# Optimization experiments

Measured on AMD Instinct MI355X. Metric: run time of the kernel, lower is better.

Reference implementation:

```python
import jax, jax.numpy as jnp
import numpy as np

K = 3
PAD = 1
STRIDE = 1
DIL = 1


def _conv(x, w, b):
    # standard 3x3 conv, NCHW / OIHW
    y = jax.lax.conv_general_dilated(
        x, w, (STRIDE, STRIDE), [(PAD, PAD), (PAD, PAD)],
        rhs_dilation=(DIL, DIL),
        dimension_numbers=('NCHW', 'OIHW', 'NCHW'))
    return y + b[None, :, None, None]


def _deform_conv2d(x, offset, mask, weight, bias):
    # x: [B,C,H,W]; offset: [B,2*KK,Ho,Wo] (y,x interleaved per kernel tap);
    # mask: [B,KK,Ho,Wo]; weight: [Co,C,K,K]; bias: [Co]
    B, C, H, W = x.shape
    KK = K * K
    Ho, Wo = offset.shape[2], offset.shape[3]

    off = offset.reshape(B, KK, 2, Ho, Wo)
    dy, dx = off[:, :, 0], off[:, :, 1]          # [B,KK,Ho,Wo]

    ky, kx = jnp.meshgrid(jnp.arange(K), jnp.arange(K), indexing='ij')
    ky = ky.reshape(KK).astype(x.dtype)
    kx = kx.reshape(KK).astype(x.dtype)
    hs = (jnp.arange(Ho) * STRIDE - PAD).astype(x.dtype)
    ws = (jnp.arange(Wo) * STRIDE - PAD).astype(x.dtype)
    base_y = hs[None, :, None] + (ky * DIL)[:, None, None]   # [KK,Ho,1]
    base_x = ws[None, None, :] + (kx * DIL)[:, None, None]   # [KK,1,Wo]

    py = base_y[None] + dy                        # [B,KK,Ho,Wo] sample rows
    px = base_x[None] + dx                        # sample cols

    y0 = jnp.floor(py)
    x0 = jnp.floor(px)
    ly = py - y0                                  # bilinear fractional weights
    lx = px - x0
    y0i = y0.astype(jnp.int32)
    x0i = x0.astype(jnp.int32)

    flat = x.reshape(B, C, H * W)

    def gather(iy, ix):
        # zero-padded gather at integer locations -> [B,C,KK,Ho,Wo]
        valid = (iy >= 0) & (iy < H) & (ix >= 0) & (ix < W)
        iyc = jnp.clip(iy, 0, H - 1)
        ixc = jnp.clip(ix, 0, W - 1)
        idx = (iyc * W + ixc).reshape(B, 1, KK * Ho * Wo)
        g = jnp.take_along_axis(flat, jnp.broadcast_to(idx, (B, C, KK * Ho * Wo)), axis=2)
        g = g.reshape(B, C, KK, Ho, Wo)
        return g * valid[:, None].astype(x.dtype)

    val = (gather(y0i, x0i) * ((1 - ly) * (1 - lx))[:, None]
           + gather(y0i, x0i + 1) * ((1 - ly) * lx)[:, None]
           + gather(y0i + 1, x0i) * (ly * (1 - lx))[:, None]
           + gather(y0i + 1, x0i + 1) * (ly * lx)[:, None])

    val = val * mask[:, None]                     # DCNv2 modulation

    wr = weight.reshape(weight.shape[0], C, KK)   # [Co,C,KK]
    out = jnp.einsum('bckhw,ock->bohw', val, wr)
    return out + bias[None, :, None, None]


def setup_inputs() -> dict:
    key = jax.random.key(0)
    ks = jax.random.split(key, 7)
    B, C, Co, H, W = 4, 128, 256, 96, 96
    KK = K * K
    x = jax.random.normal(ks[0], (B, C, H, W), dtype=jnp.float32)
    weight = jax.random.normal(ks[1], (Co, C, K, K), dtype=jnp.float32) * 0.03
    bias = jax.random.normal(ks[2], (Co,), dtype=jnp.float32) * 0.01
    offset_w = jax.random.normal(ks[3], (2 * KK, C, K, K), dtype=jnp.float32) * 0.01
    offset_b = jax.random.normal(ks[4], (2 * KK,), dtype=jnp.float32) * 0.01
    mod_w = jax.random.normal(ks[5], (KK, C, K, K), dtype=jnp.float32) * 0.01
    mod_b = jnp.ones((KK,), dtype=jnp.float32)
    return {'x': x, 'weight': weight, 'bias': bias,
            'offset_w': offset_w, 'offset_b': offset_b,
            'mod_w': mod_w, 'mod_b': mod_b}


def reference(x, weight, bias, offset_w, offset_b, mod_w, mod_b):
    offset = _conv(x, offset_w, offset_b)
    mask = jax.nn.sigmoid(_conv(x, mod_w, mod_b))
    return _deform_conv2d(x, offset, mask, weight, bias)
```

## Files before the change

kernel.cpp:

```cpp
#include <hip/hip_runtime.h>
#include <math.h>

#define HH 96
#define WW 96
#define HW 9216
#define CIN 128
#define COUT 256

typedef _Float16 f16;
typedef _Float16 f16x2 __attribute__((ext_vector_type(2)));
typedef _Float16 f16x8 __attribute__((ext_vector_type(8)));
typedef __attribute__((ext_vector_type(4))) float f32x4;

static __device__ __forceinline__ unsigned short f2h(float f) {
  union { f16 h; unsigned short u; } v; v.h = (f16)f; return v.u;
}

__global__ __launch_bounds__(256) void k_prep(const float* __restrict__ x,
                                              const float* __restrict__ offw,
                                              const float* __restrict__ modw,
                                              const float* __restrict__ wgt,
                                              unsigned short* __restrict__ xTh,
                                              unsigned short* __restrict__ wAbF,
                                              unsigned short* __restrict__ wTtF) {
  __shared__ float tile[32][129];
  int bid = blockIdx.x;
  int t = threadIdx.x;
  if (bid < 1152) {
    int wseg = bid % 3, h = (bid / 3) % 96, b = bid / 288;
    int wl = t & 31, cg = t >> 5;
    const float* xp = x + ((size_t)(b * 128 + cg) * 96 + h) * 96 + wseg * 32 + wl;
#pragma unroll
    for (int i = 0; i < 16; ++i)
      tile[wl][cg + 8 * i] = xp[(size_t)8 * i * HW];
    __syncthreads();
    int cl = t & 127, wg = t >> 7;
    unsigned short* op = xTh + (((size_t)(b * 96 + h) * 96) + wseg * 32) * 128 + cl;
#pragma unroll
    for (int i = 0; i < 16; ++i)
      op[(size_t)(wg + 2 * i) * 128] = f2h(tile[wg + 2 * i][cl]);
  } else if (bid < 1296) {
    int i = (bid - 1152) * 256 + t;
    if (i < 9 * 2 * 4 * 512) {
      int j = i & 7;
      int l = (i >> 3) & 63;
      int ks = (i >> 9) & 3;
      int ng = i >> 11;
      int kpos = ng >> 1, n16 = ng & 1;
      int n = n16 * 16 + (l & 15);
      int c = ks * 32 + (l >> 4) * 8 + j;
      float v = 0.f;
      if (n < 18) v = offw[n * 1152 + c * 9 + kpos];
      else if (n < 27) v = modw[(n - 18) * 1152 + c * 9 + kpos];
      wAbF[i] = f2h(v);
    }
  } else {
    int i = (bid - 1296) * 256 + t;
    if (i < 9 * 16 * 4 * 512) {
      int j = i & 7;
      int l = (i >> 3) & 63;
      int ks = (i >> 9) & 3;
      int ng = i >> 11;
      int kpos = ng >> 4, n16 = ng & 15;
      int n = n16 * 16 + (l & 15);
      int c = ks * 32 + (l >> 4) * 8 + j;
      wTtF[i] = f2h(wgt[n * 1152 + c * 9 + kpos]);
    }
  }
}

__global__ __launch_bounds__(256) void k_main(const unsigned short* __restrict__ xTh,
                                              const unsigned short* __restrict__ wAbF,
                                              const unsigned short* __restrict__ wTtF,
                                              const float* __restrict__ offb,
                                              const float* __restrict__ modb,
                                              const float* __restrict__ bias,
                                              float* __restrict__ out) {
  __shared__ __align__(16) unsigned short Ab[64 * 72];
  __shared__ __align__(16) float ezs[4 * 1088];
  __shared__ float om_lds[27 * 65];

  int t = threadIdx.x;
  int l = t & 63;
  int w = t >> 6;
  int lm = l & 15, lq = l >> 4;
  int raw = blockIdx.x;
  int bid = (raw & 7) * 72 + (raw >> 3);
  int pix0 = bid * 64;
  int b = pix0 / HW;
  int posim0 = pix0 % HW;
  int ibase = b * HW;

  {
    int prow = pix0 + w * 16 + lm;
    int pimo = prow % HW;
    int hoo = pimo / 96, woo = pimo % 96;
    f32x4 acco[2];
    acco[0] = (f32x4){0.f, 0.f, 0.f, 0.f};
    acco[1] = (f32x4){0.f, 0.f, 0.f, 0.f};
    const f16x8 zv = {0, 0, 0, 0, 0, 0, 0, 0};
#pragma unroll 1
    for (int kpos = 0; kpos < 9; ++kpos) {
      int dyr = kpos / 3 - 1, dxr = kpos % 3 - 1;
      bool valid = ((unsigned)(hoo + dyr) < 96u) && ((unsigned)(woo + dxr) < 96u);
      int srow = valid ? (prow + dyr * 96 + dxr) : prow;
      const unsigned short* ap = xTh + (size_t)srow * 128 + lq * 8;
      const unsigned short* bp = wAbF + (size_t)(kpos * 8) * 512 + l * 8;
#pragma unroll
      for (int ks = 0; ks < 4; ++ks) {
        f16x8 af = valid ? *(const f16x8*)(ap + ks * 32) : zv;
        f16x8 bf0 = *(const f16x8*)(bp + (size_t)ks * 512);
        f16x8 bf1 = *(const f16x8*)(bp + (size_t)(4 + ks) * 512);
        acco[0] = __builtin_amdgcn_mfma_f32_16x16x32_f16(af, bf0, acco[0], 0, 0, 0);
        acco[1] = __builtin_amdgcn_mfma_f32_16x16x32_f16(af, bf1, acco[1], 0, 0, 0);
      }
    }
#pragma unroll
    for (int nt = 0; nt < 2; ++nt) {
      int n = nt * 16 + lm;
      if (n < 27) {
        float bv = (n < 18) ? offb[n] : modb[n - 18];
#pragma unroll
        for (int r = 0; r < 4; ++r) {
          float v = acco[nt][r] + bv;
          if (n >= 18) v = 1.f / (1.f + expf(-v));
          om_lds[n * 65 + w * 16 + lq * 4 + r] = v;
        }
      }
    }
  }
  __syncthreads();

  int px = t & 63;
  int basegrp = t >> 6;
  int pos = pix0 + px;
  int ho = (pos % HW) / 96, wo = pos % 96;

  f32x4 acc[4][4];
#pragma unroll
  for (int i = 0; i < 4; ++i)
#pragma unroll
    for (int j = 0; j < 4; ++j)
      acc[i][j] = (f32x4){0.f, 0.f, 0.f, 0.f};

  for (int kpos = 0; kpos < 9; ++kpos) {
    float dy = om_lds[(2 * kpos) * 65 + px];
    float dx = om_lds[(2 * kpos + 1) * 65 + px];
    float mk = om_lds[(18 + kpos) * 65 + px];
    float py = (float)(ho - 1 + kpos / 3) + dy;
    float pxf = (float)(wo - 1 + kpos % 3) + dx;
    float fy = floorf(py), fx = floorf(pxf);
    int y0 = (int)fy, x0 = (int)fx;
    float ly = py - fy, lx = pxf - fx;
    float w00 = (1.f - ly) * (1.f - lx), w01 = (1.f - ly) * lx;
    float w10 = ly * (1.f - lx),         w11 = ly * lx;
    bool vy0 = (unsigned)y0 < 96u, vy1 = (unsigned)(y0 + 1) < 96u;
    bool vx0 = (unsigned)x0 < 96u, vx1 = (unsigned)(x0 + 1) < 96u;
    w00 = (vy0 && vx0) ? w00 * mk : 0.f;
    w01 = (vy0 && vx1) ? w01 * mk : 0.f;
    w10 = (vy1 && vx0) ? w10 * mk : 0.f;
    w11 = (vy1 && vx1) ? w11 * mk : 0.f;
    int y0c = min(max(y0, 0), 95), y1c = min(max(y0 + 1, 0), 95);
    int x0c = min(max(x0, 0), 95), x1c = min(max(x0 + 1, 0), 95);
    int o00 = (ibase + y0c * 96 + x0c) * 128;
    int o01 = (ibase + y0c * 96 + x1c) * 128;
    int o10 = (ibase + y1c * 96 + x0c) * 128;
    int o11 = (ibase + y1c * 96 + x1c) * 128;
    f16 h00 = (f16)w00, h01 = (f16)w01, h10 = (f16)w10, h11 = (f16)w11;
    f16x2 wp00 = (f16x2){h00, h00}, wp01 = (f16x2){h01, h01};
    f16x2 wp10 = (f16x2){h10, h10}, wp11 = (f16x2){h11, h11};

#pragma unroll
    for (int half = 0; half < 2; ++half) {
      int c0 = half * 64;
      __syncthreads();
#pragma unroll
      for (int item = 0; item < 2; ++item) {
        int oct = basegrp + 4 * item;
        int cc = c0 + oct * 8;
        union { uint4 u; f16x2 h[4]; } a0, a1, a2, a3;
        a0.u = *(const uint4*)(xTh + o00 + cc);
        a1.u = *(const uint4*)(xTh + o01 + cc);
        a2.u = *(const uint4*)(xTh + o10 + cc);
        a3.u = *(const uint4*)(xTh + o11 + cc);
        union { f16x8 v; f16x2 h[4]; } r;
#pragma unroll
        for (int j = 0; j < 4; ++j)
          r.h[j] = a0.h[j] * wp00 + a1.h[j] * wp01 + a2.h[j] * wp10 + a3.h[j] * wp11;
        *(f16x8*)(Ab + px * 72 + oct * 8) = r.v;
      }
      __syncthreads();
#pragma unroll
      for (int ks = 0; ks < 2; ++ks) {
        f16x8 af[4], bfv[4];
#pragma unroll
        for (int mt = 0; mt < 4; ++mt)
          af[mt] = *(const f16x8*)(Ab + (mt * 16 + lm) * 72 + ks * 32 + lq * 8);
        const unsigned short* bp =
            wTtF + (size_t)((kpos * 16 + w * 4) * 4 + 2 * half + ks) * 512 + l * 8;
#pragma unroll
        for (int nt = 0; nt < 4; ++nt)
          bfv[nt] = *(const f16x8*)(bp + (size_t)nt * 4 * 512);
#pragma unroll
        for (int mt = 0; mt < 4; ++mt)
#pragma unroll
          for (int nt = 0; nt < 4; ++nt)
            acc[mt][nt] = __builtin_amdgcn_mfma_f32_16x16x32_f16(af[mt], bfv[nt], acc[mt][nt], 0, 0, 0);
      }
    }
  }

  float bias_v[4];
#pragma unroll
  for (int nt = 0; nt < 4; ++nt) bias_v[nt] = bias[w * 64 + nt * 16 + lm];
  float* ez = ezs + w * 1088;
#pragma unroll
  for (int nt = 0; nt < 4; ++nt) {
    __syncthreads();
#pragma unroll
    for (int mt = 0; mt < 4; ++mt)
#pragma unroll
      for (int r = 0; r < 4; ++r)
        ez[(mt * 16 + lq * 4 + r) * 17 + lm] = acc[mt][nt][r] + bias_v[nt];
    __syncthreads();
    float* ob = out + ((size_t)(b * COUT + w * 64 + nt * 16)) * HW + posim0;
#pragma unroll
    for (int j = 0; j < 16; ++j)
      ob[(size_t)j * HW + l] = ez[l * 17 + j];
  }
}

extern "C" void kernel_launch(void* const* d_in, const int* in_sizes, int n_in,
                              void* d_out, int out_size, void* d_ws, size_t ws_size,
                              hipStream_t stream) {
  const float* x      = (const float*)d_in[0];
  const float* weight = (const float*)d_in[1];
  const float* bias   = (const float*)d_in[2];
  const float* offw   = (const float*)d_in[3];
  const float* offb   = (const float*)d_in[4];
  const float* modw   = (const float*)d_in[5];
  const float* modb   = (const float*)d_in[6];
  float* out = (float*)d_out;
  float* ws = (float*)d_ws;

  unsigned short* xTh  = (unsigned short*)ws;
  unsigned short* wTtF = (unsigned short*)(ws + 2359296);
  unsigned short* wAbF = (unsigned short*)(ws + 2359296 + 147456);

  k_prep<<<2448, 256, 0, stream>>>(x, offw, modw, weight, xTh, wAbF, wTtF);
  k_main<<<576, 256, 0, stream>>>(xTh, wAbF, wTtF, offb, modb, bias, out);
}
```

Measured before the change: 185.1 us.

## Register-resident A fragments with prefetched bilinear gathers per wave

Each wave now owns 16 pixels and all 256 output channels, so it builds its own A fragments in registers from the bilinear gather instead of staging a shared 64-pixel tile in LDS behind block-wide barriers. The gathers for the next kernel tap are issued before the MFMAs of the current tap, which overlaps global latency with compute. The epilogue drops most of its barriers by using a per-wave LDS transpose region. In exchange, each wave loads the full weight tile from global memory, raising weight traffic and register pressure (16 accumulators plus 16 prefetch registers) under a 2-blocks-per-CU launch bound.

```diff
diff --git a/kernel.cpp b/kernel.cpp
--- a/kernel.cpp
+++ b/kernel.cpp
@@ -69,20 +69,18 @@
   }
 }
 
-__global__ __launch_bounds__(256) void k_main(const unsigned short* __restrict__ xTh,
-                                              const unsigned short* __restrict__ wAbF,
-                                              const unsigned short* __restrict__ wTtF,
-                                              const float* __restrict__ offb,
-                                              const float* __restrict__ modb,
-                                              const float* __restrict__ bias,
-                                              float* __restrict__ out) {
-  __shared__ __align__(16) unsigned short Ab[64 * 72];
-  __shared__ __align__(16) float ezs[4 * 1088];
+__global__ __launch_bounds__(256, 2) void k_main(const unsigned short* __restrict__ xTh,
+                                                 const unsigned short* __restrict__ wAbF,
+                                                 const unsigned short* __restrict__ wTtF,
+                                                 const float* __restrict__ offb,
+                                                 const float* __restrict__ modb,
+                                                 const float* __restrict__ bias,
+                                                 float* __restrict__ out) {
   __shared__ float om_lds[27 * 65];
+  __shared__ float ez[4 * 16 * 65];
 
   int t = threadIdx.x;
-  int l = t & 63;
-  int w = t >> 6;
+  int l = t & 63, w = t >> 6;
   int lm = l & 15, lq = l >> 4;
   int raw = blockIdx.x;
   int bid = (raw & 7) * 72 + (raw >> 3);
@@ -131,24 +129,24 @@
   }
   __syncthreads();
 
-  int px = t & 63;
-  int basegrp = t >> 6;
-  int pos = pix0 + px;
-  int ho = (pos % HW) / 96, wo = pos % 96;
-
-  f32x4 acc[4][4];
-#pragma unroll
-  for (int i = 0; i < 4; ++i)
-#pragma unroll
-    for (int j = 0; j < 4; ++j)
-      acc[i][j] = (f32x4){0.f, 0.f, 0.f, 0.f};
-
-  for (int kpos = 0; kpos < 9; ++kpos) {
-    float dy = om_lds[(2 * kpos) * 65 + px];
-    float dx = om_lds[(2 * kpos + 1) * 65 + px];
-    float mk = om_lds[(18 + kpos) * 65 + px];
-    float py = (float)(ho - 1 + kpos / 3) + dy;
-    float pxf = (float)(wo - 1 + kpos % 3) + dx;
+  int mypx = w * 16 + lm;
+  int pim = (pix0 + mypx) % HW;
+  int ho = pim / 96, wo = pim % 96;
+
+  f32x4 acc[16];
+#pragma unroll
+  for (int i = 0; i < 16; ++i) acc[i] = (f32x4){0.f, 0.f, 0.f, 0.f};
+
+  int o00 = 0, o01 = 0, o10 = 0, o11 = 0;
+  f16x2 wp00, wp01, wp10, wp11;
+  uint4 q00[4], q01[4], q10[4], q11[4];
+
+  auto geom_issue = [&](int kp) {
+    float dy = om_lds[(2 * kp) * 65 + mypx];
+    float dx = om_lds[(2 * kp + 1) * 65 + mypx];
+    float mk = om_lds[(18 + kp) * 65 + mypx];
+    float py = (float)(ho - 1 + kp / 3) + dy;
+    float pxf = (float)(wo - 1 + kp % 3) + dx;
     float fy = floorf(py), fx = floorf(pxf);
     int y0 = (int)fy, x0 = (int)fx;
     float ly = py - fy, lx = pxf - fx;
@@ -162,71 +160,71 @@
     w11 = (vy1 && vx1) ? w11 * mk : 0.f;
     int y0c = min(max(y0, 0), 95), y1c = min(max(y0 + 1, 0), 95);
     int x0c = min(max(x0, 0), 95), x1c = min(max(x0 + 1, 0), 95);
-    int o00 = (ibase + y0c * 96 + x0c) * 128;
-    int o01 = (ibase + y0c * 96 + x1c) * 128;
-    int o10 = (ibase + y1c * 96 + x0c) * 128;
-    int o11 = (ibase + y1c * 96 + x1c) * 128;
+    o00 = (ibase + y0c * 96 + x0c) * 128;
+    o01 = (ibase + y0c * 96 + x1c) * 128;
+    o10 = (ibase + y1c * 96 + x0c) * 128;
+    o11 = (ibase + y1c * 96 + x1c) * 128;
     f16 h00 = (f16)w00, h01 = (f16)w01, h10 = (f16)w10, h11 = (f16)w11;
-    f16x2 wp00 = (f16x2){h00, h00}, wp01 = (f16x2){h01, h01};
-    f16x2 wp10 = (f16x2){h10, h10}, wp11 = (f16x2){h11, h11};
-
-#pragma unroll
-    for (int half = 0; half < 2; ++half) {
-      int c0 = half * 64;
-      __syncthreads();
-#pragma unroll
-      for (int item = 0; item < 2; ++item) {
-        int oct = basegrp + 4 * item;
-        int cc = c0 + oct * 8;
-        union { uint4 u; f16x2 h[4]; } a0, a1, a2, a3;
-        a0.u = *(const uint4*)(xTh + o00 + cc);
-        a1.u = *(const uint4*)(xTh + o01 + cc);
-        a2.u = *(const uint4*)(xTh + o10 + cc);
-        a3.u = *(const uint4*)(xTh + o11 + cc);
-        union { f16x8 v; f16x2 h[4]; } r;
-#pragma unroll
-        for (int j = 0; j < 4; ++j)
-          r.h[j] = a0.h[j] * wp00 + a1.h[j] * wp01 + a2.h[j] * wp10 + a3.h[j] * wp11;
-        *(f16x8*)(Ab + px * 72 + oct * 8) = r.v;
+    wp00 = (f16x2){h00, h00}; wp01 = (f16x2){h01, h01};
+    wp10 = (f16x2){h10, h10}; wp11 = (f16x2){h11, h11};
+#pragma unroll
+    for (int ks = 0; ks < 4; ++ks) {
+      int cc = ks * 32 + lq * 8;
+      q00[ks] = *(const uint4*)(xTh + o00 + cc);
+      q01[ks] = *(const uint4*)(xTh + o01 + cc);
+      q10[ks] = *(const uint4*)(xTh + o10 + cc);
+      q11[ks] = *(const uint4*)(xTh + o11 + cc);
+    }
+  };
+
+  geom_issue(0);
+
+#pragma unroll 1
+  for (int kpos = 0; kpos < 9; ++kpos) {
+    f16x8 af[4];
+    f16x2 cw00 = wp00, cw01 = wp01, cw10 = wp10, cw11 = wp11;
+#pragma unroll
+    for (int ks = 0; ks < 4; ++ks) {
+      union { uint4 u; f16x2 h[4]; } a0, a1, a2, a3;
+      a0.u = q00[ks]; a1.u = q01[ks]; a2.u = q10[ks]; a3.u = q11[ks];
+      union { f16x8 v; f16x2 h[4]; } r;
+#pragma unroll
+      for (int j = 0; j < 4; ++j)
+        r.h[j] = a0.h[j] * cw00 + a1.h[j] * cw01 + a2.h[j] * cw10 + a3.h[j] * cw11;
+      af[ks] = r.v;
+    }
+    if (kpos < 8) geom_issue(kpos + 1);
+    const unsigned short* bpk = wTtF + (size_t)(kpos * 64) * 512 + l * 8;
+#pragma unroll
+    for (int nt = 0; nt < 16; ++nt) {
+#pragma unroll
+      for (int ks = 0; ks < 4; ++ks) {
+        f16x8 bf = *(const f16x8*)(bpk + (size_t)(nt * 4 + ks) * 512);
+        acc[nt] = __builtin_amdgcn_mfma_f32_16x16x32_f16(af[ks], bf, acc[nt], 0, 0, 0);
       }
-      __syncthreads();
-#pragma unroll
-      for (int ks = 0; ks < 2; ++ks) {
-        f16x8 af[4], bfv[4];
-#pragma unroll
-        for (int mt = 0; mt < 4; ++mt)
-          af[mt] = *(const f16x8*)(Ab + (mt * 16 + lm) * 72 + ks * 32 + lq * 8);
-        const unsigned short* bp =
-            wTtF + (size_t)((kpos * 16 + w * 4) * 4 + 2 * half + ks) * 512 + l * 8;
-#pragma unroll
-        for (int nt = 0; nt < 4; ++nt)
-          bfv[nt] = *(const f16x8*)(bp + (size_t)nt * 4 * 512);
-#pragma unroll
-        for (int mt = 0; mt < 4; ++mt)
-#pragma unroll
-          for (int nt = 0; nt < 4; ++nt)
-            acc[mt][nt] = __builtin_amdgcn_mfma_f32_16x16x32_f16(af[mt], bfv[nt], acc[mt][nt], 0, 0, 0);
-      }
-    }
-  }
-
-  float bias_v[4];
-#pragma unroll
-  for (int nt = 0; nt < 4; ++nt) bias_v[nt] = bias[w * 64 + nt * 16 + lm];
-  float* ez = ezs + w * 1088;
-#pragma unroll
-  for (int nt = 0; nt < 4; ++nt) {
-    __syncthreads();
-#pragma unroll
-    for (int mt = 0; mt < 4; ++mt)
+    }
+  }
+
+  float bias_v[16];
+#pragma unroll
+  for (int nt = 0; nt < 16; ++nt) bias_v[nt] = bias[nt * 16 + lm];
+  float* z = ez + w * (16 * 65);
+  int pxr = l & 15, ng = l >> 4;
+#pragma unroll
+  for (int chunk = 0; chunk < 4; ++chunk) {
+#pragma unroll
+    for (int j = 0; j < 4; ++j) {
+      int nt = chunk * 4 + j;
 #pragma unroll
       for (int r = 0; r < 4; ++r)
-        ez[(mt * 16 + lq * 4 + r) * 17 + lm] = acc[mt][nt][r] + bias_v[nt];
-    __syncthreads();
-    float* ob = out + ((size_t)(b * COUT + w * 64 + nt * 16)) * HW + posim0;
-#pragma unroll
-    for (int j = 0; j < 16; ++j)
-      ob[(size_t)j * HW + l] = ez[l * 17 + j];
+        z[(lq * 4 + r) * 65 + j * 16 + lm] = acc[nt][r] + bias_v[nt];
+    }
+#pragma unroll
+    for (int s = 0; s < 16; ++s) {
+      int nl = s * 4 + ng;
+      out[((size_t)(b * COUT + chunk * 64 + nl)) * HW + posim0 + w * 16 + pxr] =
+          z[pxr * 65 + nl];
+    }
   }
 }
 
```

Result: slower. 271.6 us (+46.7%).
